# Performance work log

Measured on AMD Instinct MI355X. Metric: run time of the kernel, lower is better.

## Reference

```python
import jax, jax.numpy as jnp
import numpy as np

DIM = 768
NUM_HEADS = 12
WIN = (32, 32)  # pretrain window == runtime (H, W)


def _build_rel_pos_idx(wh, ww):
    coords = np.stack(np.meshgrid(np.arange(wh), np.arange(ww), indexing='ij'))  # (2,wh,ww)
    flat = coords.reshape(2, -1)  # (2, N)
    rel = flat[:, :, None] - flat[:, None, :]  # (2, N, N)
    rel = rel.transpose(1, 2, 0).astype(np.int64)  # (N, N, 2)
    rel[:, :, 0] += wh - 1
    rel[:, :, 1] += ww - 1
    rel[:, :, 0] *= 2 * ww - 1
    return rel.sum(-1)  # (N, N) in [0, (2wh-1)(2ww-1))


def setup_inputs() -> dict:
    key = jax.random.key(0)
    ks = jax.random.split(key, 7)
    wh, ww = WIN
    num_rel = (2 * wh - 1) * (2 * ww - 1) + 3  # 3972
    x = jax.random.normal(ks[0], (8, wh, ww, DIM), dtype=jnp.float32)
    qkv_w = jax.random.normal(ks[1], (3 * DIM, DIM), dtype=jnp.float32) * 0.02
    q_bias = jnp.zeros((DIM,), dtype=jnp.float32)
    v_bias = jnp.zeros((DIM,), dtype=jnp.float32)
    rel_bias_table = jax.random.normal(ks[2], (num_rel, NUM_HEADS), dtype=jnp.float32) * 0.02
    proj_w = jax.random.normal(ks[3], (DIM, DIM), dtype=jnp.float32) * 0.02
    proj_b = jnp.zeros((DIM,), dtype=jnp.float32)
    rel_pos_idx = jnp.asarray(_build_rel_pos_idx(wh, ww), dtype=jnp.int32)  # (N, N)
    return {"x": x, "qkv_w": qkv_w, "q_bias": q_bias, "v_bias": v_bias,
            "rel_bias_table": rel_bias_table, "proj_w": proj_w, "proj_b": proj_b,
            "rel_pos_idx": rel_pos_idx}


def reference(x, qkv_w, q_bias, v_bias, rel_bias_table, proj_w, proj_b, rel_pos_idx):
    B, H, W, C = x.shape
    nH = rel_bias_table.shape[-1]
    hd = C // nH
    N = H * W
    scale = hd ** -0.5
    # qkv with (q_bias, 0, v_bias) bias layout as in BEiT
    qkv_bias = jnp.concatenate([q_bias, jnp.zeros_like(v_bias), v_bias])
    qkv = x.reshape(B, N, C) @ qkv_w.T + qkv_bias  # (B, N, 3C)
    qkv = qkv.reshape(B, N, 3, nH, hd).transpose(2, 0, 3, 1, 4)  # (3, B, nH, N, hd)
    q, k, v = qkv[0], qkv[1], qkv[2]
    attn = jnp.einsum('bhnd,bhmd->bhnm', q * scale, k)  # (B, nH, N, N)
    # gathered relative-position bias: table[(N,N)] -> (N, N, nH) -> (nH, N, N)
    bias = rel_bias_table[rel_pos_idx].transpose(2, 0, 1)
    attn = jax.nn.softmax(attn + bias[None], axis=-1)
    out = jnp.einsum('bhnm,bhmd->bhnd', attn, v)  # (B, nH, N, hd)
    out = out.transpose(0, 2, 1, 3).reshape(B, H, W, C)
    return out @ proj_w.T + proj_b
```

## Files before the change

### kernel.cpp

```cpp
#include <hip/hip_runtime.h>
#include <stdint.h>

using u16 = unsigned short;
using u32 = unsigned int;

typedef __bf16 bf16x8 __attribute__((ext_vector_type(8)));
typedef float f32x4 __attribute__((ext_vector_type(4)));

__device__ __forceinline__ u16 f2bf(float f){
  u32 u = __float_as_uint(f);
  return (u16)((u + 0x7FFFu + ((u >> 16) & 1u)) >> 16);
}
__device__ __forceinline__ float bf2f(u16 h){
  return __uint_as_float(((u32)h) << 16);
}
__device__ __forceinline__ void split2(float x, u16& hi, u16& lo){
  hi = f2bf(x);
  lo = f2bf(x - bf2f(hi));
}
template<int SH>
__device__ __forceinline__ int swz(int off){ return off ^ (((off >> SH) & 7) << 4); }

__device__ __forceinline__ void gload16(const u16* g, u16* l){
  __builtin_amdgcn_global_load_lds(
      (const __attribute__((address_space(1))) void*)g,
      (__attribute__((address_space(3))) void*)l, 16, 0, 0);
}

__global__ __launch_bounds__(256) void k_split(const float* __restrict__ src,
                                               u16* __restrict__ hi,
                                               u16* __restrict__ lo)
{
  int i = blockIdx.x * 256 + threadIdx.x;
  float4 v = ((const float4*)src)[i];
  ushort4 h, l;
  split2(v.x, h.x, l.x);
  split2(v.y, h.y, l.y);
  split2(v.z, h.z, l.z);
  split2(v.w, h.w, l.w);
  ((ushort4*)hi)[i] = h;
  ((ushort4*)lo)[i] = l;
}

__global__ __launch_bounds__(256) void k_bias(const int* __restrict__ relidx,
                                              const float* __restrict__ table,
                                              u16* __restrict__ bias)
{
  int q = blockIdx.x;
  int j0 = threadIdx.x * 4;
  int4 idx = *(const int4*)(relidx + q * 1024 + j0);
#pragma unroll
  for (int h = 0; h < 12; ++h){
    ushort4 o;
    o.x = f2bf(table[(size_t)idx.x * 12 + h]);
    o.y = f2bf(table[(size_t)idx.y * 12 + h]);
    o.z = f2bf(table[(size_t)idx.z * 12 + h]);
    o.w = f2bf(table[(size_t)idx.w * 12 + h]);
    *(ushort4*)(bias + ((size_t)h << 20) + q * 1024 + j0) = o;
  }
}

__global__ __launch_bounds__(512) void k_g256(
    const u16* __restrict__ A0, const u16* __restrict__ A1, const u16* __restrict__ A2,
    const u16* __restrict__ B0, const u16* __restrict__ B1, const u16* __restrict__ B2,
    const float* __restrict__ bq, const float* __restrict__ bv,
    u16* __restrict__ QKhi, u16* __restrict__ QKlo,
    u16* __restrict__ Vthi, u16* __restrict__ Vtlo)
{
  extern __shared__ u16 R[];
  const int tid = threadIdx.x;
  const int lane = tid & 63;
  const int wid = tid >> 6;
  const int wm = wid >> 2, wn = wid & 3;
  const int g = lane >> 4, cl = lane & 15;
  const int bm = blockIdx.y << 8, bn = blockIdx.x << 8;
  const int rlane = lane >> 2;
  const int csrc = (lane & 3) ^ ((lane >> 3) & 3);

  f32x4 acc[8][4];
  f32x4 z4 = {0.f, 0.f, 0.f, 0.f};
#pragma unroll
  for (int i = 0; i < 8; ++i)
#pragma unroll
    for (int j = 0; j < 4; ++j) acc[i][j] = z4;

  auto stageA = [&](int t){
    int tt = (t < 72) ? t : t - 72;
    int ph = (tt >= 48) ? 2 : ((tt >= 24) ? 1 : 0);
    int kin = (tt - ph * 24) * 32;
    const u16* Ap = ph == 0 ? A0 : (ph == 1 ? A1 : A2);
    const int sb = (t & 3) * 16384;
#pragma unroll
    for (int i = 0; i < 2; ++i){
      int rA = (wid * 2 + i) * 16 + rlane;
      gload16(Ap + (size_t)(bm + rA) * 768 + kin + csrc * 8,
              &R[sb + (wid * 2 + i) * 512]);
    }
  };
  auto stageB = [&](int t){
    int tt = (t < 72) ? t : t - 72;
    int ph = (tt >= 48) ? 2 : ((tt >= 24) ? 1 : 0);
    int kin = (tt - ph * 24) * 32;
    const u16* Bp = ph == 0 ? B0 : (ph == 1 ? B1 : B2);
    const int sb = (t & 3) * 16384 + 8192;
#pragma unroll
    for (int i = 0; i < 2; ++i){
      int rB = (wid * 2 + i) * 16 + rlane;
      gload16(Bp + (size_t)(bn + rB) * 768 + kin + csrc * 8,
              &R[sb + (wid * 2 + i) * 512]);
    }
  };
  auto rf = [&](const u16* base, int row) -> bf16x8 {
    return *(const bf16x8*)(base + row * 32 + ((g ^ ((cl >> 1) & 3)) << 3));
  };

  stageA(0); stageB(0); stageA(1); stageB(1); stageA(2); stageB(2);

  for (int t = 0; t < 72; ++t){
    asm volatile("s_waitcnt vmcnt(8)" ::: "memory");
    __builtin_amdgcn_s_barrier();
    __builtin_amdgcn_sched_barrier(0);
    const u16* Ab = &R[(t & 3) * 16384];
    const u16* Bb = Ab + 8192;
    stageA(t + 3);
    bf16x8 bfv[4], af[4];
#pragma unroll
    for (int nf = 0; nf < 4; ++nf) bfv[nf] = rf(Bb, wn * 64 + nf * 16 + cl);
#pragma unroll
    for (int mf = 0; mf < 4; ++mf) af[mf] = rf(Ab, wm * 128 + mf * 16 + cl);
    asm volatile("s_waitcnt lgkmcnt(0)" ::: "memory");
    __builtin_amdgcn_sched_barrier(0);
    __builtin_amdgcn_s_setprio(1);
#pragma unroll
    for (int mf = 0; mf < 4; ++mf)
#pragma unroll
      for (int nf = 0; nf < 4; ++nf)
        acc[mf][nf] = __builtin_amdgcn_mfma_f32_16x16x32_bf16(af[mf], bfv[nf], acc[mf][nf], 0, 0, 0);
    __builtin_amdgcn_s_setprio(0);
    __builtin_amdgcn_s_barrier();
    __builtin_amdgcn_sched_barrier(0);
    stageB(t + 3);
#pragma unroll
    for (int mf = 0; mf < 4; ++mf) af[mf] = rf(Ab, wm * 128 + (mf + 4) * 16 + cl);
    asm volatile("s_waitcnt lgkmcnt(0)" ::: "memory");
    __builtin_amdgcn_sched_barrier(0);
    __builtin_amdgcn_s_setprio(1);
#pragma unroll
    for (int mf = 0; mf < 4; ++mf)
#pragma unroll
      for (int nf = 0; nf < 4; ++nf)
        acc[mf + 4][nf] = __builtin_amdgcn_mfma_f32_16x16x32_bf16(af[mf], bfv[nf], acc[mf + 4][nf], 0, 0, 0);
    __builtin_amdgcn_s_setprio(0);
  }

  const int bb = bm >> 10;
  const int tokb = bm & 1023;
  u16* Hs = R;
  u16* Ls = R + 8192;

  if (blockIdx.x < 6){
    const bool isQ = (blockIdx.x < 3);
#pragma unroll
    for (int c = 0; c < 8; ++c){
      __syncthreads();
      if (wm == (c >> 2)){
#pragma unroll
        for (int mi = 0; mi < 2; ++mi){
          const int mf = (c & 3) * 2 + mi;
#pragma unroll
          for (int nf = 0; nf < 4; ++nf){
            int col = wn * 64 + nf * 16 + cl;
            float bqv = isQ ? bq[bn + col] : 0.f;
#pragma unroll
            for (int r = 0; r < 4; ++r){
              float v = acc[mf][nf][r];
              if (isQ) v = (v + bqv) * 0.125f;
              u16 hi, lo; split2(v, hi, lo);
              int idx = (mi * 16 + g * 4 + r) * 256 + col;
              Hs[idx] = hi;
              Ls[idx] = lo;
            }
          }
        }
      }
      __syncthreads();
#pragma unroll
      for (int i = 0; i < 2; ++i){
        int s = tid + i * 512;
        int rr = s >> 5, seg = s & 31;
        size_t gb = (size_t)(bm + c * 32 + rr) * 1536 + bn + seg * 8;
        *(float4*)(QKhi + gb) = *(const float4*)(Hs + rr * 256 + seg * 8);
        *(float4*)(QKlo + gb) = *(const float4*)(Ls + rr * 256 + seg * 8);
      }
    }
  } else {
    const int ccolbase = bn - 1536;
#pragma unroll
    for (int c = 0; c < 8; ++c){
      __syncthreads();
      if (wn == (c >> 1)){
#pragma unroll
        for (int nf2 = 0; nf2 < 2; ++nf2){
          const int nf = (c & 1) * 2 + nf2;
          int cc = nf2 * 16 + cl;
          float bvv = bv[ccolbase + c * 32 + cc];
#pragma unroll
          for (int mf = 0; mf < 8; ++mf){
            ushort4 h4, l4;
            u16 hh_, ll_;
            split2(acc[mf][nf][0] + bvv, hh_, ll_); h4.x = hh_; l4.x = ll_;
            split2(acc[mf][nf][1] + bvv, hh_, ll_); h4.y = hh_; l4.y = ll_;
            split2(acc[mf][nf][2] + bvv, hh_, ll_); h4.z = hh_; l4.z = ll_;
            split2(acc[mf][nf][3] + bvv, hh_, ll_); h4.w = hh_; l4.w = ll_;
            int m0 = wm * 128 + mf * 16 + g * 4;
            int off = cc * 512 + m0 * 2;
            *(ushort4*)((char*)Hs + swz<9>(off)) = h4;
            *(ushort4*)((char*)Ls + swz<9>(off)) = l4;
          }
        }
      }
      __syncthreads();
#pragma unroll
      for (int i = 0; i < 2; ++i){
        int s = tid + i * 512;
        int dr = s >> 5, seg = s & 31;
        int off = dr * 512 + seg * 16;
        int ccol = ccolbase + c * 32 + dr;
        int hh = ccol >> 6, d = ccol & 63;
        size_t gb = ((size_t)(bb * 12 + hh) * 64 + d) * 1024 + tokb + seg * 8;
        *(float4*)(Vthi + gb) = *(const float4*)((char*)Hs + swz<9>(off));
        *(float4*)(Vtlo + gb) = *(const float4*)((char*)Ls + swz<9>(off));
      }
    }
  }
}

template<int EPI>
__global__ __launch_bounds__(256) void k_gemm(
    const u16* __restrict__ A0, const u16* __restrict__ A1, const u16* __restrict__ A2,
    const u16* __restrict__ B0, const u16* __restrict__ B1, const u16* __restrict__ B2,
    const float* __restrict__ pb,
    float* __restrict__ Cout)
{
  __shared__ __align__(16) u16 As[4][128 * 32];
  __shared__ __align__(16) u16 Bs[4][128 * 32];
  const int tid = threadIdx.x;
  const int lane = tid & 63;
  const int wid = tid >> 6;
  const int wr = wid >> 1, wc = wid & 1;
  const int g = lane >> 4, cl = lane & 15;
  const int bm = blockIdx.y << 7, bn = blockIdx.x << 7;
  const int srow = lane >> 2;
  const int sseg = ((lane & 3) ^ ((lane >> 3) & 3)) * 8;
  const int gph  = (g ^ ((cl >> 1) & 3)) * 8;

  f32x4 acc[4][4];
  f32x4 z4 = {0.f, 0.f, 0.f, 0.f};
#pragma unroll
  for (int i = 0; i < 4; ++i)
#pragma unroll
    for (int j = 0; j < 4; ++j) acc[i][j] = z4;

  auto stage = [&](int t){
    int tt = (t < 72) ? t : t - 72;
    int ph = (tt >= 48) ? 2 : ((tt >= 24) ? 1 : 0);
    int kin = (tt - ph * 24) * 32;
    const u16* Ap = ph == 0 ? A0 : (ph == 1 ? A1 : A2);
    const u16* Bp = ph == 0 ? B0 : (ph == 1 ? B1 : B2);
    const int slot = t & 3;
#pragma unroll
    for (int c = 0; c < 2; ++c){
      int chunk = wid * 2 + c;
      int row = chunk * 16 + srow;
      gload16(Ap + (size_t)(bm + row) * 768 + kin + sseg, &As[slot][chunk * 512]);
      gload16(Bp + (size_t)(bn + row) * 768 + kin + sseg, &Bs[slot][chunk * 512]);
    }
  };

  stage(0); stage(1); stage(2);
  for (int t = 0; t < 72; ++t){
    asm volatile("s_waitcnt vmcnt(8)" ::: "memory");
    __builtin_amdgcn_s_barrier();
    __builtin_amdgcn_sched_barrier(0);
    stage(t + 3);
    const int slot = t & 3;
    bf16x8 af[4], bfv[4];
#pragma unroll
    for (int mf = 0; mf < 4; ++mf)
      af[mf] = *(const bf16x8*)(&As[slot][(wr * 64 + mf * 16 + cl) * 32 + gph]);
#pragma unroll
    for (int nf = 0; nf < 4; ++nf)
      bfv[nf] = *(const bf16x8*)(&Bs[slot][(wc * 64 + nf * 16 + cl) * 32 + gph]);
#pragma unroll
    for (int mf = 0; mf < 4; ++mf)
#pragma unroll
      for (int nf = 0; nf < 4; ++nf)
        acc[mf][nf] = __builtin_amdgcn_mfma_f32_16x16x32_bf16(af[mf], bfv[nf], acc[mf][nf], 0, 0, 0);
  }

  __syncthreads();
#pragma unroll
  for (int mf = 0; mf < 4; ++mf)
#pragma unroll
    for (int nf = 0; nf < 4; ++nf)
#pragma unroll
      for (int r = 0; r < 4; ++r){
        int m = bm + wr * 64 + mf * 16 + g * 4 + r;
        int n = bn + wc * 64 + nf * 16 + cl;
        Cout[(size_t)m * 768 + n] = acc[mf][nf][r] + pb[n];
      }
}

__global__ __launch_bounds__(256) void k_attn(
    const u16* __restrict__ QKhi, const u16* __restrict__ QKlo,
    const u16* __restrict__ Vthi, const u16* __restrict__ Vtlo,
    const u16* __restrict__ bias,
    u16* __restrict__ Ohi, u16* __restrict__ Olo)
{
  __shared__ __align__(16) u16 lds[36864];
  const int KH0 = 0, KL0 = 8192, VH0 = 16384, VL0 = 24576, PS = 32768;

  const int tid = threadIdx.x;
  const int lane = tid & 63;
  const int w = tid >> 6;
  const int g = lane >> 4, cl = lane & 15;
  const int qt = blockIdx.x;
  const int b  = blockIdx.y;
  const int h  = blockIdx.z;
  const size_t rowbase = (size_t)b * 1024;
  const size_t bhv = (size_t)(b * 12 + h) * (1024 * 64);
  const u16* bias_w = bias + ((size_t)h << 20) + (size_t)(qt * 64 + w * 16) * 1024;

  const int dr = lane >> 3, dc = lane & 7;
  const int csrc = dc ^ dr;
  const size_t kbase = (rowbase + w * 16 + dr) * 1536 + 768 + (size_t)h * 64 + csrc * 8;
  const size_t vbase = bhv + (size_t)(w * 16 + dr) * 1024 + csrc * 8;

  auto stage = [&](int buf, int jt){
#pragma unroll
    for (int i = 0; i < 2; ++i){
      int r0 = (w * 16 + i * 8) * 64;
      size_t ko = kbase + (size_t)(jt * 64 + i * 8) * 1536;
      size_t vo = vbase + (size_t)i * 8 * 1024 + jt * 64;
      gload16(QKhi + ko, &lds[KH0 + buf * 4096 + r0]);
      gload16(QKlo + ko, &lds[KL0 + buf * 4096 + r0]);
      gload16(Vthi + vo, &lds[VH0 + buf * 4096 + r0]);
      gload16(Vtlo + vo, &lds[VL0 + buf * 4096 + r0]);
    }
  };
  auto tread = [&](int base, int r, int cb) -> bf16x8 {
    int byte = r * 128 + ((cb ^ (r & 7)) << 4);
    return *(const bf16x8*)((const char*)&lds[base] + byte);
  };

  bf16x8 aq[4];
  {
    const u16* qh = QKhi + (rowbase + qt * 64 + w * 16 + cl) * 1536 + h * 64;
    const u16* ql = QKlo + (rowbase + qt * 64 + w * 16 + cl) * 1536 + h * 64;
    aq[0] = *(const bf16x8*)(qh + g * 8);
    aq[1] = *(const bf16x8*)(qh + 32 + g * 8);
    aq[2] = *(const bf16x8*)(ql + g * 8);
    aq[3] = *(const bf16x8*)(ql + 32 + g * 8);
  }

  f32x4 o[4];
  float m_run[4], l_run[4];
  f32x4 z4 = {0.f, 0.f, 0.f, 0.f};
#pragma unroll
  for (int nd = 0; nd < 4; ++nd) o[nd] = z4;
#pragma unroll
  for (int r = 0; r < 4; ++r){ m_run[r] = -1e30f; l_run[r] = 0.f; }

  const int AI[6] = {0, 1, 0, 1, 2, 3};
  const int BI[6] = {0, 1, 2, 3, 0, 1};

  stage(0, 0);
  int buf = 0;
  for (int jt = 0; jt < 16; ++jt){
    __syncthreads();
    if (jt + 1 < 16) stage(buf ^ 1, jt + 1);

    f32x4 s[4];
#pragma unroll
    for (int nf = 0; nf < 4; ++nf) s[nf] = z4;
#pragma unroll
    for (int ks = 0; ks < 6; ++ks){
      const int t = BI[ks];
      const int kb = (t >= 2 ? KL0 : KH0) + buf * 4096;
      const int cb = (t & 1) * 4 + g;
      bf16x8 b4[4];
#pragma unroll
      for (int nf = 0; nf < 4; ++nf)
        b4[nf] = tread(kb, nf * 16 + cl, cb);
#pragma unroll
      for (int nf = 0; nf < 4; ++nf)
        s[nf] = __builtin_amdgcn_mfma_f32_16x16x32_bf16(aq[AI[ks]], b4[nf], s[nf], 0, 0, 0);
    }

#pragma unroll
    for (int nf = 0; nf < 4; ++nf){
      int jc = jt * 64 + nf * 16 + cl;
#pragma unroll
      for (int r = 0; r < 4; ++r)
        s[nf][r] += bf2f(bias_w[(size_t)(g * 4 + r) * 1024 + jc]);
    }
#pragma unroll
    for (int r = 0; r < 4; ++r){
      float mx = fmaxf(fmaxf(s[0][r], s[1][r]), fmaxf(s[2][r], s[3][r]));
      mx = fmaxf(mx, __shfl_xor(mx, 1));
      mx = fmaxf(mx, __shfl_xor(mx, 2));
      mx = fmaxf(mx, __shfl_xor(mx, 4));
      mx = fmaxf(mx, __shfl_xor(mx, 8));
      float mn = fmaxf(m_run[r], mx);
      float fs = __expf(m_run[r] - mn);
      m_run[r] = mn;
      float rs = 0.f;
#pragma unroll
      for (int nf = 0; nf < 4; ++nf){
        float p = __expf(s[nf][r] - mn);
        s[nf][r] = p;
        rs += p;
      }
      rs += __shfl_xor(rs, 1);
      rs += __shfl_xor(rs, 2);
      rs += __shfl_xor(rs, 4);
      rs += __shfl_xor(rs, 8);
      l_run[r] = l_run[r] * fs + rs;
#pragma unroll
      for (int nd = 0; nd < 4; ++nd) o[nd][r] *= fs;
    }
#pragma unroll
    for (int nf = 0; nf < 4; ++nf)
#pragma unroll
      for (int r = 0; r < 4; ++r){
        int off = (w * 16 + g * 4 + r) * 128 + (nf * 16 + cl) * 2;
        *(u16*)((char*)&lds[PS] + swz<7>(off)) = f2bf(s[nf][r]);
      }

    bf16x8 pa[2];
    {
      int row = (w * 16 + cl) * 128;
      pa[0] = *(const bf16x8*)((char*)&lds[PS] + swz<7>(row + (g * 8) * 2));
      pa[1] = *(const bf16x8*)((char*)&lds[PS] + swz<7>(row + (32 + g * 8) * 2));
    }
#pragma unroll
    for (int ks = 0; ks < 4; ++ks){
      const int vb = (ks < 2 ? VH0 : VL0) + buf * 4096;
      const int cb = (ks & 1) * 4 + g;
      bf16x8 b4[4];
#pragma unroll
      for (int nd = 0; nd < 4; ++nd)
        b4[nd] = tread(vb, nd * 16 + cl, cb);
#pragma unroll
      for (int nd = 0; nd < 4; ++nd)
        o[nd] = __builtin_amdgcn_mfma_f32_16x16x32_bf16(pa[ks & 1], b4[nd], o[nd], 0, 0, 0);
    }
    buf ^= 1;
  }

  __syncthreads();
#pragma unroll
  for (int r = 0; r < 4; ++r){
    float inv = 1.f / l_run[r];
    int row = w * 16 + g * 4 + r;
#pragma unroll
    for (int nd = 0; nd < 4; ++nd){
      u16 hi, lo; split2(o[nd][r] * inv, hi, lo);
      int off = row * 128 + (nd * 16 + cl) * 2;
      *(u16*)((char*)&lds[PS]  + swz<7>(off)) = hi;
      *(u16*)((char*)&lds[KH0] + swz<7>(off)) = lo;
    }
  }
  __syncthreads();
#pragma unroll
  for (int i = 0; i < 2; ++i){
    int s = tid + i * 256;
    int qr = s >> 3;
    int seg = s & 7;
    int off = qr * 128 + seg * 16;
    size_t gb = ((size_t)b * 1024 + qt * 64 + qr) * 768 + h * 64 + seg * 8;
    *(float4*)(Ohi + gb) = *(const float4*)((char*)&lds[PS]  + swz<7>(off));
    *(float4*)(Olo + gb) = *(const float4*)((char*)&lds[KH0] + swz<7>(off));
  }
}

extern "C" void kernel_launch(void* const* d_in, const int* in_sizes, int n_in,
                              void* d_out, int out_size, void* d_ws, size_t ws_size,
                              hipStream_t stream)
{
  const float* x      = (const float*)d_in[0];
  const float* qkv_w  = (const float*)d_in[1];
  const float* q_bias = (const float*)d_in[2];
  const float* v_bias = (const float*)d_in[3];
  const float* table  = (const float*)d_in[4];
  const float* proj_w = (const float*)d_in[5];
  const float* proj_b = (const float*)d_in[6];
  const int*   relidx = (const int*)d_in[7];
  float* out = (float*)d_out;

  char* ws = (char*)d_ws;
  size_t off = 0;
  auto alloc = [&](size_t nelem) -> u16* {
    u16* p = (u16*)(ws + off);
    off += (nelem * 2 + 255) & ~(size_t)255;
    return p;
  };
  u16* Xhi  = alloc((size_t)8192 * 768);
  u16* Xlo  = alloc((size_t)8192 * 768);
  u16* Whi  = alloc((size_t)2304 * 768);
  u16* Wlo  = alloc((size_t)2304 * 768);
  u16* PWhi = alloc((size_t)768 * 768);
  u16* PWlo = alloc((size_t)768 * 768);
  u16* QKhi = alloc((size_t)8192 * 1536);
  u16* QKlo = alloc((size_t)8192 * 1536);
  u16* Vthi = alloc((size_t)8 * 12 * 64 * 1024);
  u16* Vtlo = alloc((size_t)8 * 12 * 64 * 1024);
  u16* Bias = alloc((size_t)12 * 1024 * 1024);
  u16* Ohi = Xhi;
  u16* Olo = Xlo;

  k_split<<<6144, 256, 0, stream>>>(x, Xhi, Xlo);
  k_split<<<1728, 256, 0, stream>>>(qkv_w, Whi, Wlo);
  k_split<<<576,  256, 0, stream>>>(proj_w, PWhi, PWlo);
  k_bias<<<1024, 256, 0, stream>>>(relidx, table, Bias);

  k_g256<<<dim3(9, 32), 512, 131072, stream>>>(
      Xhi, Xhi, Xlo, Whi, Wlo, Whi,
      q_bias, v_bias,
      QKhi, QKlo, Vthi, Vtlo);

  k_attn<<<dim3(16, 8, 12), 256, 0, stream>>>(
      QKhi, QKlo, Vthi, Vtlo, Bias, Ohi, Olo);

  k_gemm<1><<<dim3(6, 64), 256, 0, stream>>>(
      Ohi, Ohi, Olo, PWhi, PWlo, PWhi,
      proj_b, out);
}
```

Baseline: 438.2 us.

## Rework QKV and projection GEMM pipelines with 64-wide K tiles and XCD block remap

Both GEMM kernels switch from 4-stage 32-wide K staging to 2-stage double-buffered 64-wide K tiles with a row-xor swizzle, halving loop iterations and barrier count. Blocks are remapped so consecutive tiles land on the same XCD for better L2 reuse. The trade-off is shallower prefetch depth and reliance on __syncthreads for load completion instead of explicit partial vmcnt waits.

```diff
diff --git a/kernel.cpp b/kernel.cpp
--- a/kernel.cpp
+++ b/kernel.cpp
@@ -73,9 +73,13 @@
   const int wid = tid >> 6;
   const int wm = wid >> 2, wn = wid & 3;
   const int g = lane >> 4, cl = lane & 15;
-  const int bm = blockIdx.y << 8, bn = blockIdx.x << 8;
-  const int rlane = lane >> 2;
-  const int csrc = (lane & 3) ^ ((lane >> 3) & 3);
+  const int orig = blockIdx.y * gridDim.x + blockIdx.x;
+  const int cpx = (gridDim.x * gridDim.y) >> 3;
+  const int wg = (orig & 7) * cpx + (orig >> 3);
+  const int bx = wg % gridDim.x, by = wg / gridDim.x;
+  const int bm = by << 8, bn = bx << 8;
+  const int dr = lane >> 3, dc = lane & 7;
+  const int csrc = dc ^ dr;
 
   f32x4 acc[8][4];
   f32x4 z4 = {0.f, 0.f, 0.f, 0.f};
@@ -84,73 +88,54 @@
 #pragma unroll
     for (int j = 0; j < 4; ++j) acc[i][j] = z4;
 
-  auto stageA = [&](int t){
-    int tt = (t < 72) ? t : t - 72;
-    int ph = (tt >= 48) ? 2 : ((tt >= 24) ? 1 : 0);
-    int kin = (tt - ph * 24) * 32;
+  auto stage = [&](int t){
+    if (t >= 36) return;
+    int ph = t / 12;
+    int kin = (t - ph * 12) * 64;
     const u16* Ap = ph == 0 ? A0 : (ph == 1 ? A1 : A2);
-    const int sb = (t & 3) * 16384;
-#pragma unroll
-    for (int i = 0; i < 2; ++i){
-      int rA = (wid * 2 + i) * 16 + rlane;
-      gload16(Ap + (size_t)(bm + rA) * 768 + kin + csrc * 8,
-              &R[sb + (wid * 2 + i) * 512]);
-    }
-  };
-  auto stageB = [&](int t){
-    int tt = (t < 72) ? t : t - 72;
-    int ph = (tt >= 48) ? 2 : ((tt >= 24) ? 1 : 0);
-    int kin = (tt - ph * 24) * 32;
     const u16* Bp = ph == 0 ? B0 : (ph == 1 ? B1 : B2);
-    const int sb = (t & 3) * 16384 + 8192;
-#pragma unroll
-    for (int i = 0; i < 2; ++i){
-      int rB = (wid * 2 + i) * 16 + rlane;
-      gload16(Bp + (size_t)(bn + rB) * 768 + kin + csrc * 8,
-              &R[sb + (wid * 2 + i) * 512]);
-    }
-  };
-  auto rf = [&](const u16* base, int row) -> bf16x8 {
-    return *(const bf16x8*)(base + row * 32 + ((g ^ ((cl >> 1) & 3)) << 3));
-  };
-
-  stageA(0); stageB(0); stageA(1); stageB(1); stageA(2); stageB(2);
-
-  for (int t = 0; t < 72; ++t){
-    asm volatile("s_waitcnt vmcnt(8)" ::: "memory");
-    __builtin_amdgcn_s_barrier();
-    __builtin_amdgcn_sched_barrier(0);
-    const u16* Ab = &R[(t & 3) * 16384];
-    const u16* Bb = Ab + 8192;
-    stageA(t + 3);
-    bf16x8 bfv[4], af[4];
-#pragma unroll
-    for (int nf = 0; nf < 4; ++nf) bfv[nf] = rf(Bb, wn * 64 + nf * 16 + cl);
-#pragma unroll
-    for (int mf = 0; mf < 4; ++mf) af[mf] = rf(Ab, wm * 128 + mf * 16 + cl);
-    asm volatile("s_waitcnt lgkmcnt(0)" ::: "memory");
-    __builtin_amdgcn_sched_barrier(0);
-    __builtin_amdgcn_s_setprio(1);
-#pragma unroll
-    for (int mf = 0; mf < 4; ++mf)
+    const int sb = (t & 1) * 32768;
+#pragma unroll
+    for (int c = 0; c < 4; ++c){
+      int row = wid * 32 + c * 8;
+      gload16(Ap + (size_t)(bm + row + dr) * 768 + kin + csrc * 8,
+              &R[sb + row * 64]);
+      gload16(Bp + (size_t)(bn + row + dr) * 768 + kin + csrc * 8,
+              &R[sb + 16384 + row * 64]);
+    }
+  };
+  auto rf = [&](const u16* base, int row, int lc) -> bf16x8 {
+    return *(const bf16x8*)(base + row * 64 + ((lc ^ (row & 7)) << 3));
+  };
+
+  stage(0);
+  for (int t = 0; t < 36; ++t){
+    __syncthreads();
+    stage(t + 1);
+    const u16* Ab = &R[(t & 1) * 32768];
+    const u16* Bb = Ab + 16384;
+#pragma unroll
+    for (int ks = 0; ks < 2; ++ks){
+      bf16x8 bfv[4];
 #pragma unroll
       for (int nf = 0; nf < 4; ++nf)
-        acc[mf][nf] = __builtin_amdgcn_mfma_f32_16x16x32_bf16(af[mf], bfv[nf], acc[mf][nf], 0, 0, 0);
-    __builtin_amdgcn_s_setprio(0);
-    __builtin_amdgcn_s_barrier();
-    __builtin_amdgcn_sched_barrier(0);
-    stageB(t + 3);
-#pragma unroll
-    for (int mf = 0; mf < 4; ++mf) af[mf] = rf(Ab, wm * 128 + (mf + 4) * 16 + cl);
-    asm volatile("s_waitcnt lgkmcnt(0)" ::: "memory");
-    __builtin_amdgcn_sched_barrier(0);
-    __builtin_amdgcn_s_setprio(1);
-#pragma unroll
-    for (int mf = 0; mf < 4; ++mf)
-#pragma unroll
-      for (int nf = 0; nf < 4; ++nf)
-        acc[mf + 4][nf] = __builtin_amdgcn_mfma_f32_16x16x32_bf16(af[mf], bfv[nf], acc[mf + 4][nf], 0, 0, 0);
-    __builtin_amdgcn_s_setprio(0);
+        bfv[nf] = rf(Bb, wn * 64 + nf * 16 + cl, ks * 4 + g);
+      __builtin_amdgcn_s_setprio(1);
+#pragma unroll
+      for (int half = 0; half < 2; ++half){
+        bf16x8 af[4];
+#pragma unroll
+        for (int mf = 0; mf < 4; ++mf)
+          af[mf] = rf(Ab, wm * 128 + (half * 4 + mf) * 16 + cl, ks * 4 + g);
+#pragma unroll
+        for (int mf = 0; mf < 4; ++mf)
+#pragma unroll
+          for (int nf = 0; nf < 4; ++nf)
+            acc[half * 4 + mf][nf] =
+                __builtin_amdgcn_mfma_f32_16x16x32_bf16(af[mf], bfv[nf], acc[half * 4 + mf][nf], 0, 0, 0);
+      }
+      __builtin_amdgcn_s_setprio(0);
+    }
   }
 
   const int bb = bm >> 10;
@@ -158,8 +143,8 @@
   u16* Hs = R;
   u16* Ls = R + 8192;
 
-  if (blockIdx.x < 6){
-    const bool isQ = (blockIdx.x < 3);
+  if (bx < 6){
+    const bool isQ = (bx < 3);
 #pragma unroll
     for (int c = 0; c < 8; ++c){
       __syncthreads();
@@ -223,9 +208,9 @@
 #pragma unroll
       for (int i = 0; i < 2; ++i){
         int s = tid + i * 512;
-        int dr = s >> 5, seg = s & 31;
-        int off = dr * 512 + seg * 16;
-        int ccol = ccolbase + c * 32 + dr;
+        int drr = s >> 5, seg = s & 31;
+        int off = drr * 512 + seg * 16;
+        int ccol = ccolbase + c * 32 + drr;
         int hh = ccol >> 6, d = ccol & 63;
         size_t gb = ((size_t)(bb * 12 + hh) * 64 + d) * 1024 + tokb + seg * 8;
         *(float4*)(Vthi + gb) = *(const float4*)((char*)Hs + swz<9>(off));
@@ -235,24 +220,25 @@
   }
 }
 
-template<int EPI>
-__global__ __launch_bounds__(256) void k_gemm(
+__global__ __launch_bounds__(256) void k_proj(
     const u16* __restrict__ A0, const u16* __restrict__ A1, const u16* __restrict__ A2,
     const u16* __restrict__ B0, const u16* __restrict__ B1, const u16* __restrict__ B2,
     const float* __restrict__ pb,
     float* __restrict__ Cout)
 {
-  __shared__ __align__(16) u16 As[4][128 * 32];
-  __shared__ __align__(16) u16 Bs[4][128 * 32];
+  __shared__ __align__(16) u16 R[2][16384];
   const int tid = threadIdx.x;
   const int lane = tid & 63;
   const int wid = tid >> 6;
   const int wr = wid >> 1, wc = wid & 1;
   const int g = lane >> 4, cl = lane & 15;
-  const int bm = blockIdx.y << 7, bn = blockIdx.x << 7;
-  const int srow = lane >> 2;
-  const int sseg = ((lane & 3) ^ ((lane >> 3) & 3)) * 8;
-  const int gph  = (g ^ ((cl >> 1) & 3)) * 8;
+  const int orig = blockIdx.y * gridDim.x + blockIdx.x;
+  const int cpx = (gridDim.x * gridDim.y) >> 3;
+  const int wg = (orig & 7) * cpx + (orig >> 3);
+  const int bx = wg % gridDim.x, by = wg / gridDim.x;
+  const int bm = by << 7, bn = bx << 7;
+  const int dr = lane >> 3, dc = lane & 7;
+  const int csrc = dc ^ dr;
 
   f32x4 acc[4][4];
   f32x4 z4 = {0.f, 0.f, 0.f, 0.f};
@@ -262,43 +248,48 @@
     for (int j = 0; j < 4; ++j) acc[i][j] = z4;
 
   auto stage = [&](int t){
-    int tt = (t < 72) ? t : t - 72;
-    int ph = (tt >= 48) ? 2 : ((tt >= 24) ? 1 : 0);
-    int kin = (tt - ph * 24) * 32;
+    if (t >= 36) return;
+    int ph = t / 12;
+    int kin = (t - ph * 12) * 64;
     const u16* Ap = ph == 0 ? A0 : (ph == 1 ? A1 : A2);
     const u16* Bp = ph == 0 ? B0 : (ph == 1 ? B1 : B2);
-    const int slot = t & 3;
-#pragma unroll
-    for (int c = 0; c < 2; ++c){
-      int chunk = wid * 2 + c;
-      int row = chunk * 16 + srow;
-      gload16(Ap + (size_t)(bm + row) * 768 + kin + sseg, &As[slot][chunk * 512]);
-      gload16(Bp + (size_t)(bn + row) * 768 + kin + sseg, &Bs[slot][chunk * 512]);
-    }
-  };
-
-  stage(0); stage(1); stage(2);
-  for (int t = 0; t < 72; ++t){
-    asm volatile("s_waitcnt vmcnt(8)" ::: "memory");
-    __builtin_amdgcn_s_barrier();
-    __builtin_amdgcn_sched_barrier(0);
-    stage(t + 3);
-    const int slot = t & 3;
-    bf16x8 af[4], bfv[4];
-#pragma unroll
-    for (int mf = 0; mf < 4; ++mf)
-      af[mf] = *(const bf16x8*)(&As[slot][(wr * 64 + mf * 16 + cl) * 32 + gph]);
-#pragma unroll
-    for (int nf = 0; nf < 4; ++nf)
-      bfv[nf] = *(const bf16x8*)(&Bs[slot][(wc * 64 + nf * 16 + cl) * 32 + gph]);
-#pragma unroll
-    for (int mf = 0; mf < 4; ++mf)
+    u16* S = R[t & 1];
+#pragma unroll
+    for (int c = 0; c < 4; ++c){
+      int row = wid * 32 + c * 8;
+      gload16(Ap + (size_t)(bm + row + dr) * 768 + kin + csrc * 8, S + row * 64);
+      gload16(Bp + (size_t)(bn + row + dr) * 768 + kin + csrc * 8, S + 8192 + row * 64);
+    }
+  };
+  auto rf = [&](const u16* base, int row, int lc) -> bf16x8 {
+    return *(const bf16x8*)(base + row * 64 + ((lc ^ (row & 7)) << 3));
+  };
+
+  stage(0);
+  for (int t = 0; t < 36; ++t){
+    __syncthreads();
+    stage(t + 1);
+    const u16* Ab = R[t & 1];
+    const u16* Bb = Ab + 8192;
+#pragma unroll
+    for (int ks = 0; ks < 2; ++ks){
+      bf16x8 bfv[4], af[4];
 #pragma unroll
       for (int nf = 0; nf < 4; ++nf)
-        acc[mf][nf] = __builtin_amdgcn_mfma_f32_16x16x32_bf16(af[mf], bfv[nf], acc[mf][nf], 0, 0, 0);
-  }
-
-  __syncthreads();
+        bfv[nf] = rf(Bb, wc * 64 + nf * 16 + cl, ks * 4 + g);
+#pragma unroll
+      for (int mf = 0; mf < 4; ++mf)
+        af[mf] = rf(Ab, wr * 64 + mf * 16 + cl, ks * 4 + g);
+      __builtin_amdgcn_s_setprio(1);
+#pragma unroll
+      for (int mf = 0; mf < 4; ++mf)
+#pragma unroll
+        for (int nf = 0; nf < 4; ++nf)
+          acc[mf][nf] = __builtin_amdgcn_mfma_f32_16x16x32_bf16(af[mf], bfv[nf], acc[mf][nf], 0, 0, 0);
+      __builtin_amdgcn_s_setprio(0);
+    }
+  }
+
 #pragma unroll
   for (int mf = 0; mf < 4; ++mf)
 #pragma unroll
@@ -532,7 +523,7 @@
   k_attn<<<dim3(16, 8, 12), 256, 0, stream>>>(
       QKhi, QKlo, Vthi, Vtlo, Bias, Ohi, Olo);
 
-  k_gemm<1><<<dim3(6, 64), 256, 0, stream>>>(
+  k_proj<<<dim3(6, 64), 256, 0, stream>>>(
       Ohi, Ohi, Olo, PWhi, PWlo, PWhi,
       proj_b, out);
 }
```

Result: slower. 576.5 us (+31.6%).
